# Optimization experiments

Measured on AMD Instinct MI355X. Metric: run time of the kernel, lower is better.

Reference implementation:

```python
import jax, jax.numpy as jnp
import numpy as np

C = 256
CQK = C // 8  # 32


def setup_inputs() -> dict:
    key = jax.random.key(0)
    ks = jax.random.split(key, 8)
    B, H, W = 4, 64, 64
    x = jax.random.normal(ks[0], (B, H, W, C), dtype=jnp.float32)
    # 1x1 conv weights == dense projections over channel dim
    Wf = jax.random.normal(ks[1], (C, CQK), dtype=jnp.float32) * (1.0 / np.sqrt(C))
    bf = jnp.zeros((CQK,), dtype=jnp.float32)
    Wg = jax.random.normal(ks[2], (C, CQK), dtype=jnp.float32) * (1.0 / np.sqrt(C))
    bg = jnp.zeros((CQK,), dtype=jnp.float32)
    Wh = jax.random.normal(ks[3], (C, C), dtype=jnp.float32) * (1.0 / np.sqrt(C))
    bh = jnp.zeros((C,), dtype=jnp.float32)
    gamma = jnp.float32(0.5)  # nonzero so attention path contributes
    return {"x": x, "Wf": Wf, "bf": bf, "Wg": Wg, "bg": bg, "Wh": Wh, "bh": bh, "gamma": gamma}


def reference(x, Wf, bf, Wg, bg, Wh, bh, gamma):
    B, H, W, Cc = x.shape
    N = H * W
    xf = x.reshape(B, N, Cc)                       # hw_flatten
    f = xf @ Wf + bf                               # [B, N, C//8] keys
    g = xf @ Wg + bg                               # [B, N, C//8] queries
    h = xf @ Wh + bh                               # [B, N, C] values
    s = jnp.einsum('bnc,bmc->bnm', g, f)           # [B, N, N]
    b = jax.nn.softmax(s, axis=-1)
    o = jnp.einsum('bnm,bmc->bnc', b, h)           # [B, N, C]
    y = gamma * o.reshape(B, H, W, Cc) + x
    return y
```

## Files before the change

### kernel.cpp

```cpp
#include <hip/hip_runtime.h>
#include <hip/hip_bf16.h>

#define BATCH 4
#define NSEQ  4096
#define CDIM  256
#define CQK   32
#define L2E   1.44269504088896340736f

typedef short bf16x8 __attribute__((ext_vector_type(8)));
typedef float f32x16 __attribute__((ext_vector_type(16)));
typedef unsigned short u16;
typedef unsigned int   u32;
typedef unsigned int   u32x4 __attribute__((ext_vector_type(4)));

__device__ __forceinline__ u32 pk2(float lo, float hi) {
  u16 a = __builtin_bit_cast(u16, __float2bfloat16(lo));
  u16 b = __builtin_bit_cast(u16, __float2bfloat16(hi));
  return (u32)a | ((u32)b << 16);
}
__device__ __forceinline__ bf16x8 ld8(const u16* p) {
  uint4 u = *(const uint4*)p;
  return __builtin_bit_cast(bf16x8, u);
}
__device__ __forceinline__ float exp2_raw(float x) {
#if __has_builtin(__builtin_amdgcn_exp2f)
  return __builtin_amdgcn_exp2f(x);
#else
  return exp2f(x);
#endif
}

__global__ __launch_bounds__(64) void prep_kernel(
    const float* __restrict__ Wf, const float* __restrict__ Wg, const float* __restrict__ Wh,
    u16* __restrict__ wfT, u16* __restrict__ wgT, u16* __restrict__ whT) {
  const int cb = blockIdx.x, t = threadIdx.x;
#pragma unroll
  for (int j = 0; j < 4; ++j) {
    const int k = t + j * 64;
    if (cb < 32) {
      wfT[cb * 256 + k] = (u16)(pk2(Wf[k * CQK + cb] * L2E, 0.f) & 0xFFFF);
    } else if (cb < 64) {
      const int c = cb - 32;
      wgT[c * 256 + k] = (u16)(pk2(Wg[k * CQK + c], 0.f) & 0xFFFF);
    } else {
      const int c = cb - 64;
      whT[c * 256 + k] = (u16)(pk2(Wh[k * CDIM + c], 0.f) & 0xFFFF);
    }
  }
}

__global__ __launch_bounds__(256, 2) void proj_kernel(
    const float* __restrict__ x,
    const float* __restrict__ bfv, const float* __restrict__ bgv, const float* __restrict__ bhv,
    const u16* __restrict__ wfT, const u16* __restrict__ wgT, const u16* __restrict__ whT,
    u16* __restrict__ fP, u16* __restrict__ g_ws, u16* __restrict__ hP) {
  const int tid   = threadIdx.x;
  const int lan   = tid & 63;
  const int lan31 = lan & 31;
  const int g2    = lan >> 5;
  const int w     = tid >> 6;
  const int row0  = blockIdx.x * 32;
  const int b     = row0 >> 12;
  const int kcg   = row0 >> 5;

  bf16x8 xf[16];
  const float* xr = x + ((size_t)row0 + lan31) * CDIM + g2 * 8;
#pragma unroll
  for (int ks = 0; ks < 16; ++ks) {
    float4 a = *(const float4*)(xr + ks * 16);
    float4 c = *(const float4*)(xr + ks * 16 + 4);
    u32x4 u = { pk2(a.x, a.y), pk2(a.z, a.w), pk2(c.x, c.y), pk2(c.z, c.w) };
    xf[ks] = __builtin_bit_cast(bf16x8, u);
  }

  if (w < 2) {
    const u16*  wT   = w ? wgT : wfT;
    const float bias = w ? bgv[lan31] : bfv[lan31] * L2E;
    f32x16 acc;
#pragma unroll
    for (int r = 0; r < 16; ++r) acc[r] = bias;
    const u16* wp = wT + lan31 * 256 + g2 * 8;
#pragma unroll
    for (int ks = 0; ks < 16; ++ks)
      acc = __builtin_amdgcn_mfma_f32_32x32x16_bf16(xf[ks], ld8(wp + ks * 16), acc, 0, 0, 0);
    if (w) {
#pragma unroll
      for (int r = 0; r < 16; ++r) {
        const int row = (r & 3) + 8 * (r >> 2) + 4 * g2;
        g_ws[((size_t)row0 + row) * CQK + lan31] = (u16)(pk2(acc[r], 0.f) & 0xFFFF);
      }
    } else {
      u16* fb = fP + (size_t)kcg * 1024
              + (lan31 >> 4) * 512 + ((lan31 >> 3) & 1) * 256 + (lan31 & 7);
#pragma unroll
      for (int r = 0; r < 16; ++r) {
        const int crow = (r & 3) + 8 * (r >> 2) + 4 * g2;
        fb[crow * 8] = (u16)(pk2(acc[r], 0.f) & 0xFFFF);
      }
    }
  }

#pragma unroll
  for (int t = 0; t < 2; ++t) {
    const int cg = w * 2 + t;
    const int ct = cg * 32;
    f32x16 acc;
#pragma unroll
    for (int r = 0; r < 16; ++r)
      acc[r] = bhv[ct + (r & 3) + 8 * (r >> 2) + 4 * g2];
    const u16* wp = whT + (size_t)(ct + lan31) * 256 + g2 * 8;
#pragma unroll
    for (int ks = 0; ks < 16; ++ks)
      acc = __builtin_amdgcn_mfma_f32_32x32x16_bf16(ld8(wp + ks * 16), xf[ks], acc, 0, 0, 0);
    u16* hb = hP + ((size_t)(b * 8 + cg) * 128 + ((row0 & (NSEQ - 1)) >> 5)) * 1024
            + (lan31 >> 4) * 512 + ((lan31 >> 3) & 1) * 256 + (lan31 & 7);
#pragma unroll
    for (int r = 0; r < 16; ++r) {
      const int crow = (r & 3) + 8 * (r >> 2) + 4 * g2;
      hb[crow * 8] = (u16)(pk2(acc[r], 0.f) & 0xFFFF);
    }
  }
}

__global__ __launch_bounds__(256, 2) void attn_kernel(
    const float* __restrict__ x, const float* __restrict__ gamma_p,
    const u16* __restrict__ fP, const u16* __restrict__ g_ws,
    const u16* __restrict__ hP, float* __restrict__ out) {
  __shared__ u32   pls[4][2][2][16][64];
  __shared__ float lsh[4][2][64];

  const int tid   = threadIdx.x;
  const int lan   = tid & 63;
  const int lan31 = lan & 31;
  const int g2    = lan >> 5;
  const int kw    = tid >> 6;
  const int bid   = blockIdx.x;
  const int xcd   = bid & 7;
  const int b     = xcd >> 1;
  const int inner = bid >> 3;
  const int cb    = inner & 1;
  const int n0    = ((((xcd & 1) << 5) | (inner >> 1))) * 64;

  const float gamma = gamma_p[0];

  bf16x8 bgM[2][2];
#pragma unroll
  for (int qh = 0; qh < 2; ++qh) {
    const u16* gp = g_ws + ((size_t)b * NSEQ + n0 + qh * 32 + lan31) * CQK + g2 * 8;
    bgM[qh][0] = ld8(gp);
    bgM[qh][1] = ld8(gp + 16);
  }

  f32x16 o[4][2], zfrag;
#pragma unroll
  for (int r = 0; r < 16; ++r) zfrag[r] = 0.f;
#pragma unroll
  for (int cg = 0; cg < 4; ++cg) { o[cg][0] = zfrag; o[cg][1] = zfrag; }
  float l2[2] = {0.f, 0.f};

  const u16*  fpk = fP + (size_t)(b * 128 + kw * 32) * 1024 + lan * 8;
  const u16*  hpk = hP + ((size_t)(b * 8 + cb * 4) * 128 + kw * 32) * 1024 + lan * 8;
  const size_t hcg = (size_t)128 * 1024;

  bf16x8 af0 = ld8(fpk), af1 = ld8(fpk + 512);
  fpk += 1024;

  for (int it = 0; it < 32; ++it) {
    bf16x8 naf0 = ld8(fpk), naf1 = ld8(fpk + 512);
    fpk += 1024;
    bf16x8 ha[4], hb[4];
#pragma unroll
    for (int cg = 0; cg < 4; ++cg) {
      ha[cg] = ld8(hpk + cg * hcg);
      hb[cg] = ld8(hpk + cg * hcg + 512);
    }
    hpk += 1024;

#pragma unroll
    for (int qh = 0; qh < 2; ++qh) {
      f32x16 s = __builtin_amdgcn_mfma_f32_32x32x16_bf16(af0, bgM[qh][0], zfrag, 0, 0, 0);
      s        = __builtin_amdgcn_mfma_f32_32x32x16_bf16(af1, bgM[qh][1], s,     0, 0, 0);

      float pv[16];
#pragma unroll
      for (int r = 0; r < 16; ++r) pv[r] = exp2_raw(s[r]);
      float rs = ((pv[0]+pv[1])+(pv[2]+pv[3])) + ((pv[4]+pv[5])+(pv[6]+pv[7]))
               + ((pv[8]+pv[9])+(pv[10]+pv[11])) + ((pv[12]+pv[13])+(pv[14]+pv[15]));
      auto rr = __builtin_amdgcn_permlane32_swap(__builtin_bit_cast(u32, rs),
                                                 __builtin_bit_cast(u32, rs), false, false);
      l2[qh] += __builtin_bit_cast(float, (u32)rr[0]) + __builtin_bit_cast(float, (u32)rr[1]);

      u32 q0a = pk2(pv[0],pv[1]),   q0b = pk2(pv[2],pv[3]);
      u32 q1a = pk2(pv[4],pv[5]),   q1b = pk2(pv[6],pv[7]);
      u32 q2a = pk2(pv[8],pv[9]),   q2b = pk2(pv[10],pv[11]);
      u32 q3a = pk2(pv[12],pv[13]), q3b = pk2(pv[14],pv[15]);
      auto r02a = __builtin_amdgcn_permlane32_swap(q0a, q1a, false, false);
      auto r13a = __builtin_amdgcn_permlane32_swap(q0b, q1b, false, false);
      auto r02b = __builtin_amdgcn_permlane32_swap(q2a, q3a, false, false);
      auto r13b = __builtin_amdgcn_permlane32_swap(q2b, q3b, false, false);
      u32x4 u0 = {(u32)r02a[0], (u32)r13a[0], (u32)r02a[1], (u32)r13a[1]};
      u32x4 u1 = {(u32)r02b[0], (u32)r13b[0], (u32)r02b[1], (u32)r13b[1]};
      bf16x8 ap0 = __builtin_bit_cast(bf16x8, u0);
      bf16x8 ap1 = __builtin_bit_cast(bf16x8, u1);

#pragma unroll
      for (int cg = 0; cg < 4; ++cg) {
        o[cg][qh] = __builtin_amdgcn_mfma_f32_32x32x16_bf16(ap0, ha[cg], o[cg][qh], 0, 0, 0);
        o[cg][qh] = __builtin_amdgcn_mfma_f32_32x32x16_bf16(ap1, hb[cg], o[cg][qh], 0, 0, 0);
      }
    }

    af0 = naf0; af1 = naf1;
  }

  lsh[kw][0][lan] = l2[0];
  lsh[kw][1][lan] = l2[1];
#pragma unroll
  for (int cgp = 0; cgp < 2; ++cgp)
#pragma unroll
    for (int qh = 0; qh < 2; ++qh)
#pragma unroll
      for (int r = 0; r < 16; ++r)
        pls[kw][cgp][qh][r][lan] = pk2(o[cgp * 2][qh][r], o[cgp * 2 + 1][qh][r]);
  __syncthreads();

  const int cgp = kw >> 1, qh = kw & 1;
  float e0[16], e1[16];
#pragma unroll
  for (int r = 0; r < 16; ++r) { e0[r] = 0.f; e1[r] = 0.f; }
#pragma unroll
  for (int kk = 0; kk < 4; ++kk)
#pragma unroll
    for (int r = 0; r < 16; ++r) {
      u32 v = pls[kk][cgp][qh][r][lan];
      e0[r] += __builtin_bit_cast(float, v << 16);
      e1[r] += __builtin_bit_cast(float, v & 0xFFFF0000u);
    }
  const float l_tot = lsh[0][qh][lan] + lsh[1][qh][lan]
                    + lsh[2][qh][lan] + lsh[3][qh][lan];
  const float gi = gamma / l_tot;
#pragma unroll
  for (int r = 0; r < 16; ++r) {
    const int nl = (r & 3) + 8 * (r >> 2) + 4 * g2;
    const float gir = __shfl(gi, nl);
    const size_t row = (size_t)b * NSEQ + n0 + qh * 32 + nl;
    const size_t i0 = row * CDIM + cb * 128 + cgp * 64 + lan31;
    out[i0]      = fmaf(gir, e0[r], x[i0]);
    out[i0 + 32] = fmaf(gir, e1[r], x[i0 + 32]);
  }
}

extern "C" void kernel_launch(void* const* d_in, const int* in_sizes, int n_in,
                              void* d_out, int out_size, void* d_ws, size_t ws_size,
                              hipStream_t stream) {
  const float* x     = (const float*)d_in[0];
  const float* Wf    = (const float*)d_in[1];
  const float* bf    = (const float*)d_in[2];
  const float* Wg    = (const float*)d_in[3];
  const float* bg    = (const float*)d_in[4];
  const float* Wh    = (const float*)d_in[5];
  const float* bh    = (const float*)d_in[6];
  const float* gamma = (const float*)d_in[7];
  float* out = (float*)d_out;

  u16* hP   = (u16*)d_ws;
  u16* fPp  = hP  + (size_t)BATCH * CDIM * NSEQ;
  u16* g_ws = fPp + (size_t)BATCH * NSEQ * CQK;
  u16* wfT  = g_ws + (size_t)BATCH * NSEQ * CQK;
  u16* wgT  = wfT + (size_t)CQK * CDIM;
  u16* whT  = wgT + (size_t)CQK * CDIM;

  hipLaunchKernelGGL(prep_kernel, dim3(320), dim3(64), 0, stream,
                     Wf, Wg, Wh, wfT, wgT, whT);
  hipLaunchKernelGGL(proj_kernel, dim3(512), dim3(256), 0, stream,
                     x, bf, bg, bh, wfT, wgT, whT, fPp, g_ws, hP);
  hipLaunchKernelGGL(attn_kernel, dim3(512), dim3(256), 0, stream,
                     x, gamma, fPp, g_ws, hP, out);
}
```

Baseline: 80.46 us.

## Software-pipeline softmax of next key tile with PV MFMAs of current tile

Restructures the attention inner loop so the QK MFMA, exp2, bf16 packing and permlane shuffles for tile i+1 are issued before the PV MFMAs for tile i. The aim is to overlap the transcendental and VALU work with MFMA execution rather than running them in a serial chain. Value (h) fragments are now loaded two at a time, interleaved with the MFMAs, instead of all eight up front, which cuts register pressure and spreads memory latency. The cost is one wasted softmax step on the final iteration (its row-sum is skipped) and an extra key prefetch that reads one tile past the original loop's range.

```diff
diff --git a/kernel.cpp b/kernel.cpp
--- a/kernel.cpp
+++ b/kernel.cpp
@@ -162,34 +162,24 @@
   const u16*  hpk = hP + ((size_t)(b * 8 + cb * 4) * 128 + kw * 32) * 1024 + lan * 8;
   const size_t hcg = (size_t)128 * 1024;
 
-  bf16x8 af0 = ld8(fpk), af1 = ld8(fpk + 512);
-  fpk += 1024;
-
-  for (int it = 0; it < 32; ++it) {
-    bf16x8 naf0 = ld8(fpk), naf1 = ld8(fpk + 512);
-    fpk += 1024;
-    bf16x8 ha[4], hb[4];
-#pragma unroll
-    for (int cg = 0; cg < 4; ++cg) {
-      ha[cg] = ld8(hpk + cg * hcg);
-      hb[cg] = ld8(hpk + cg * hcg + 512);
-    }
-    hpk += 1024;
-
+  bf16x8 af0, af1;
+  bf16x8 apc[2][2], apn[2][2];
+
+  auto sm_step = [&](bool do_l, bf16x8 (&dst)[2][2]) {
 #pragma unroll
     for (int qh = 0; qh < 2; ++qh) {
       f32x16 s = __builtin_amdgcn_mfma_f32_32x32x16_bf16(af0, bgM[qh][0], zfrag, 0, 0, 0);
       s        = __builtin_amdgcn_mfma_f32_32x32x16_bf16(af1, bgM[qh][1], s,     0, 0, 0);
-
       float pv[16];
 #pragma unroll
       for (int r = 0; r < 16; ++r) pv[r] = exp2_raw(s[r]);
-      float rs = ((pv[0]+pv[1])+(pv[2]+pv[3])) + ((pv[4]+pv[5])+(pv[6]+pv[7]))
-               + ((pv[8]+pv[9])+(pv[10]+pv[11])) + ((pv[12]+pv[13])+(pv[14]+pv[15]));
-      auto rr = __builtin_amdgcn_permlane32_swap(__builtin_bit_cast(u32, rs),
-                                                 __builtin_bit_cast(u32, rs), false, false);
-      l2[qh] += __builtin_bit_cast(float, (u32)rr[0]) + __builtin_bit_cast(float, (u32)rr[1]);
-
+      if (do_l) {
+        float rs = ((pv[0]+pv[1])+(pv[2]+pv[3])) + ((pv[4]+pv[5])+(pv[6]+pv[7]))
+                 + ((pv[8]+pv[9])+(pv[10]+pv[11])) + ((pv[12]+pv[13])+(pv[14]+pv[15]));
+        auto rr = __builtin_amdgcn_permlane32_swap(__builtin_bit_cast(u32, rs),
+                                                   __builtin_bit_cast(u32, rs), false, false);
+        l2[qh] += __builtin_bit_cast(float, (u32)rr[0]) + __builtin_bit_cast(float, (u32)rr[1]);
+      }
       u32 q0a = pk2(pv[0],pv[1]),   q0b = pk2(pv[2],pv[3]);
       u32 q1a = pk2(pv[4],pv[5]),   q1b = pk2(pv[6],pv[7]);
       u32 q2a = pk2(pv[8],pv[9]),   q2b = pk2(pv[10],pv[11]);
@@ -200,17 +190,48 @@
       auto r13b = __builtin_amdgcn_permlane32_swap(q2b, q3b, false, false);
       u32x4 u0 = {(u32)r02a[0], (u32)r13a[0], (u32)r02a[1], (u32)r13a[1]};
       u32x4 u1 = {(u32)r02b[0], (u32)r13b[0], (u32)r02b[1], (u32)r13b[1]};
-      bf16x8 ap0 = __builtin_bit_cast(bf16x8, u0);
-      bf16x8 ap1 = __builtin_bit_cast(bf16x8, u1);
-
-#pragma unroll
-      for (int cg = 0; cg < 4; ++cg) {
-        o[cg][qh] = __builtin_amdgcn_mfma_f32_32x32x16_bf16(ap0, ha[cg], o[cg][qh], 0, 0, 0);
-        o[cg][qh] = __builtin_amdgcn_mfma_f32_32x32x16_bf16(ap1, hb[cg], o[cg][qh], 0, 0, 0);
-      }
-    }
-
-    af0 = naf0; af1 = naf1;
+      dst[qh][0] = __builtin_bit_cast(bf16x8, u0);
+      dst[qh][1] = __builtin_bit_cast(bf16x8, u1);
+    }
+  };
+
+  af0 = ld8(fpk); af1 = ld8(fpk + 512); fpk += 1024;
+  sm_step(true, apc);
+  af0 = ld8(fpk); af1 = ld8(fpk + 512); fpk += 1024;
+
+  for (int it = 0; it < 32; ++it) {
+    bf16x8 hA0 = ld8(hpk),       hA1 = ld8(hpk + 512);
+
+    sm_step(it < 31, apn);
+
+    af0 = ld8(fpk); af1 = ld8(fpk + 512); fpk += 1024;
+
+    bf16x8 hB0 = ld8(hpk + hcg), hB1 = ld8(hpk + hcg + 512);
+
+    o[0][0] = __builtin_amdgcn_mfma_f32_32x32x16_bf16(apc[0][0], hA0, o[0][0], 0, 0, 0);
+    o[0][0] = __builtin_amdgcn_mfma_f32_32x32x16_bf16(apc[0][1], hA1, o[0][0], 0, 0, 0);
+    o[0][1] = __builtin_amdgcn_mfma_f32_32x32x16_bf16(apc[1][0], hA0, o[0][1], 0, 0, 0);
+    o[0][1] = __builtin_amdgcn_mfma_f32_32x32x16_bf16(apc[1][1], hA1, o[0][1], 0, 0, 0);
+    hA0 = ld8(hpk + 2 * hcg); hA1 = ld8(hpk + 2 * hcg + 512);
+
+    o[1][0] = __builtin_amdgcn_mfma_f32_32x32x16_bf16(apc[0][0], hB0, o[1][0], 0, 0, 0);
+    o[1][0] = __builtin_amdgcn_mfma_f32_32x32x16_bf16(apc[0][1], hB1, o[1][0], 0, 0, 0);
+    o[1][1] = __builtin_amdgcn_mfma_f32_32x32x16_bf16(apc[1][0], hB0, o[1][1], 0, 0, 0);
+    o[1][1] = __builtin_amdgcn_mfma_f32_32x32x16_bf16(apc[1][1], hB1, o[1][1], 0, 0, 0);
+    hB0 = ld8(hpk + 3 * hcg); hB1 = ld8(hpk + 3 * hcg + 512);
+
+    o[2][0] = __builtin_amdgcn_mfma_f32_32x32x16_bf16(apc[0][0], hA0, o[2][0], 0, 0, 0);
+    o[2][0] = __builtin_amdgcn_mfma_f32_32x32x16_bf16(apc[0][1], hA1, o[2][0], 0, 0, 0);
+    o[2][1] = __builtin_amdgcn_mfma_f32_32x32x16_bf16(apc[1][0], hA0, o[2][1], 0, 0, 0);
+    o[2][1] = __builtin_amdgcn_mfma_f32_32x32x16_bf16(apc[1][1], hA1, o[2][1], 0, 0, 0);
+    o[3][0] = __builtin_amdgcn_mfma_f32_32x32x16_bf16(apc[0][0], hB0, o[3][0], 0, 0, 0);
+    o[3][0] = __builtin_amdgcn_mfma_f32_32x32x16_bf16(apc[0][1], hB1, o[3][0], 0, 0, 0);
+    o[3][1] = __builtin_amdgcn_mfma_f32_32x32x16_bf16(apc[1][0], hB0, o[3][1], 0, 0, 0);
+    o[3][1] = __builtin_amdgcn_mfma_f32_32x32x16_bf16(apc[1][1], hB1, o[3][1], 0, 0, 0);
+
+    hpk += 1024;
+    apc[0][0] = apn[0][0]; apc[0][1] = apn[0][1];
+    apc[1][0] = apn[1][0]; apc[1][1] = apn[1][1];
   }
 
   lsh[kw][0][lan] = l2[0];
```

After: 90.28 us. 1.12x slower.
